# Performance work log

Hardware: AMD Instinct MI355X
Metric: run time of the kernel (lower is better)

The kernel has to match this reference:

```python
import jax, jax.numpy as jnp
import numpy as np

N_NODES = 500_000
N_EDGES = 1_000_000
EMB = 64           # config.Model.embedding_size
F = 128            # config.Model.latency_feature_size
L = 8              # config.Latency.latency_feature_length
OP_CNT = 5000
SV_CNT = 2000
ST_CNT = 16
IN_DIM = 3 * EMB + L  # 200


def setup_inputs() -> dict:
    key = jax.random.key(0)
    ks = jax.random.split(key, 24)
    s = 0.02
    inp = {
        'operation_id': jax.random.randint(ks[0], (N_NODES,), 0, OP_CNT, dtype=jnp.int32),
        'service_id':   jax.random.randint(ks[1], (N_NODES,), 0, SV_CNT, dtype=jnp.int32),
        'status_id':    jax.random.randint(ks[2], (N_NODES,), 0, ST_CNT, dtype=jnp.int32),
        'latency_feat': jax.random.normal(ks[3], (N_NODES, L), dtype=jnp.float32),
        'edge_src':     jax.random.randint(ks[4], (N_EDGES,), 0, N_NODES, dtype=jnp.int32),
        'edge_dst':     jax.random.randint(ks[5], (N_EDGES,), 0, N_NODES, dtype=jnp.int32),
        'eps':          jax.random.normal(ks[6], (N_NODES, F), dtype=jnp.float32),
        # parameters (LevelEmbedding + TreeLSTMLatencyEncoder + TreeLSTMLatencyDecoder)
        'op_embed':      jax.random.normal(ks[7],  (OP_CNT, EMB), dtype=jnp.float32) * s,
        'service_embed': jax.random.normal(ks[8],  (SV_CNT, EMB), dtype=jnp.float32) * s,
        'status_embed':  jax.random.normal(ks[9],  (ST_CNT, EMB), dtype=jnp.float32) * s,
        'enc_W1': jax.random.normal(ks[10], (IN_DIM, F), dtype=jnp.float32) * s,
        'enc_b1': jnp.zeros((F,), dtype=jnp.float32),
        'enc_W2': jax.random.normal(ks[11], (F, 2 * F), dtype=jnp.float32) * s,
        'enc_b2': jnp.zeros((2 * F,), dtype=jnp.float32),
        'dec_Wself': jax.random.normal(ks[12], (F, F), dtype=jnp.float32) * s,
        'dec_Wagg':  jax.random.normal(ks[13], (F, F), dtype=jnp.float32) * s,
        'mu_W': jax.random.normal(ks[14], (F, L), dtype=jnp.float32) * s,
        'mu_b': jnp.zeros((L,), dtype=jnp.float32),
        'lv_W': jax.random.normal(ks[15], (F, L), dtype=jnp.float32) * s,
        'lv_b': jnp.zeros((L,), dtype=jnp.float32),
        'opwise_embed': jax.random.normal(ks[16], (OP_CNT + 1, 2 * L * L), dtype=jnp.float32) * s,
    }
    return inp


def reference(operation_id, service_id, status_id, latency_feat, edge_src, edge_dst, eps,
              op_embed, service_embed, status_embed,
              enc_W1, enc_b1, enc_W2, enc_b2,
              dec_Wself, dec_Wagg, mu_W, mu_b, lv_W, lv_b, opwise_embed):
    N = latency_feat.shape[0]
    # ---- LevelEmbedding: gathers + concat ----
    feats = jnp.concatenate([
        op_embed[operation_id],
        service_embed[service_id],
        status_embed[status_id],
        latency_feat,
    ], axis=-1)  # [N, 3*EMB + L]
    # ---- TreeLSTMLatencyEncoder ----
    h = jax.nn.relu(feats @ enc_W1 + enc_b1)
    y = h @ enc_W2 + enc_b2                       # [N, 2F]
    z_mu, z_lv = jnp.split(y, 2, axis=-1)
    z_lv = jnp.tanh(z_lv)
    z = z_mu + jnp.exp(0.5 * z_lv) * eps          # reparameterize, [N, F]
    # ---- TreeLSTM decoder (one child-sum message-passing step over edges) ----
    agg = jax.ops.segment_sum(z[edge_src], edge_dst, num_segments=N)  # scatter-reduce
    yd = jax.nn.relu(z @ dec_Wself + agg @ dec_Wagg)                  # [N, F]
    mu = yd @ mu_W + mu_b   # [N, L]
    lv = yd @ lv_W + lv_b   # [N, L]
    # op-wise output transform: per-node [1,L] @ [L,L]
    w = opwise_embed[operation_id].reshape(N, L, 2 * L)
    w_mu, w_lv = w[..., :L], w[..., L:]
    mu = jnp.einsum('nl,nlk->nk', mu, w_mu)
    lv = jnp.einsum('nl,nlk->nk', lv, w_lv)
    # ---- latency_loss: gaussian NLL + opid scatter aggregation ----
    label = latency_feat
    loss = (mu - label) ** 2 / (2.0 * jnp.exp(lv) + 1e-7) + 0.5 * lv  # [N, L]
    loss_node = jnp.mean(loss, axis=1)                                 # [N]
    op_loss = jax.ops.segment_sum(loss_node, operation_id, num_segments=OP_CNT)
    op_cnt = jax.ops.segment_sum(jnp.ones((N,), jnp.int32), operation_id, num_segments=OP_CNT)
    lat_loss = jnp.mean(loss_node)
    kl = -0.5 * jnp.mean(z_lv + 1.0 - jnp.exp(z_lv) - z_mu ** 2)
    total = lat_loss + kl
    return (total, op_loss, op_cnt)
```

## Files before the change

kernel.cpp:

```cpp
#include <hip/hip_runtime.h>
#include <math.h>

#define NN 500000
#define NE 1000000
#define OPC 5000
#define NBLK_SCAN 489
#define NBLK ((NN + 127) / 128)

typedef short short8 __attribute__((ext_vector_type(8)));
typedef float f32x4 __attribute__((ext_vector_type(4)));

static __device__ __forceinline__ short f2bf(float f) {
    unsigned u = __builtin_bit_cast(unsigned, f);
    u += 0x7fffu + ((u >> 16) & 1u);
    return (short)(u >> 16);
}
static __device__ __forceinline__ float bf2f(short s) {
    unsigned u = ((unsigned)(unsigned short)s) << 16;
    return __builtin_bit_cast(float, u);
}
static __device__ __forceinline__ short8 cvt8(float4 a, float4 b) {
    short8 r;
    r[0] = f2bf(a.x); r[1] = f2bf(a.y); r[2] = f2bf(a.z); r[3] = f2bf(a.w);
    r[4] = f2bf(b.x); r[5] = f2bf(b.y); r[6] = f2bf(b.z); r[7] = f2bf(b.w);
    return r;
}
static __device__ __forceinline__ short8 ldcvt(const float* p) {
    const float4* p4 = (const float4*)p;
    return cvt8(p4[0], p4[1]);
}

__global__ void prep_kernel(const float* __restrict__ W1, const float* __restrict__ W2,
                            const float* __restrict__ Wself, const float* __restrict__ Wagg,
                            const float* __restrict__ muW, const float* __restrict__ lvW,
                            short* __restrict__ W1f, short* __restrict__ W2f,
                            short* __restrict__ Wf0, short* __restrict__ Wf1,
                            short* __restrict__ HWf)
{
    int idx = blockIdx.x * 256 + threadIdx.x;
    int j = idx & 7, lane = (idx >> 3) & 63;
    int m = lane & 15, q = lane >> 4;
    {
        int s = idx >> 12, nf = (idx >> 9) & 7;
        int k = s * 32 + q * 8 + j, col = nf * 16 + m;
        W1f[idx] = (k < 200) ? f2bf(W1[k * 128 + col]) : (short)0;
    }
    {
        int s = idx >> 13, nf = (idx >> 9) & 15;
        int k = s * 32 + q * 8 + j, col = nf * 16 + m;
        W2f[idx] = f2bf(W2[k * 256 + col]);
    }
    if (idx < 16384) {
        int s = idx >> 12, nf = (idx >> 9) & 7;
        int k = s * 32 + q * 8 + j, col = nf * 16 + m;
        Wf0[idx] = f2bf(Wself[k * 128 + col]);
        Wf1[idx] = f2bf(Wagg[k * 128 + col]);
    }
    if (idx < 2048) {
        int k = (idx >> 9) * 32 + q * 8 + j;
        HWf[idx] = (m < 8) ? f2bf(muW[k * 8 + m]) : f2bf(lvW[k * 8 + (m - 8)]);
    }
}

__global__ __launch_bounds__(256, 4) void enc1_mfma(
    const int* __restrict__ op_id, const int* __restrict__ sv_id, const int* __restrict__ st_id,
    const float* __restrict__ lat,
    const float* __restrict__ opE, const float* __restrict__ svE, const float* __restrict__ stE,
    const short* __restrict__ W1f, const float* __restrict__ b1,
    short* __restrict__ h_bf)
{
    __shared__ __align__(16) short Hs[128 * 136];
    const int tid = threadIdx.x;
    const int lane = tid & 63, w = tid >> 6;
    const int m = lane & 15, q = lane >> 4;
    const int bbase = blockIdx.x * 128;
    const int wbase = bbase + w * 32;
    const bool wv = (wbase < NN);

    #pragma unroll
    for (int a2 = 0; a2 < 2; a2++) {
        if (wv) {
            const int n0 = wbase + a2 * 16 + m;
            const size_t op0 = (size_t)op_id[n0] * 64;
            const size_t sv0 = (size_t)sv_id[n0] * 64;
            const size_t st0 = (size_t)st_id[n0] * 64;

            f32x4 acc[8];
            #pragma unroll
            for (int nf = 0; nf < 8; nf++) acc[nf] = (f32x4)0.0f;

            #pragma unroll
            for (int s = 0; s < 7; s++) {
                short8 a0;
                if (s < 2)      a0 = ldcvt(opE + op0 + s * 32 + q * 8);
                else if (s < 4) a0 = ldcvt(svE + sv0 + (s - 2) * 32 + q * 8);
                else if (s < 6) a0 = ldcvt(stE + st0 + (s - 4) * 32 + q * 8);
                else {
                    if (q == 0) a0 = ldcvt(lat + (size_t)n0 * 8);
                    else {
                        #pragma unroll
                        for (int i = 0; i < 8; i++) a0[i] = 0;
                    }
                }
                #pragma unroll
                for (int nf = 0; nf < 8; nf++) {
                    const short8 b = *(const short8*)(W1f + (s * 8 + nf) * 512 + lane * 8);
                    acc[nf] = __builtin_amdgcn_mfma_f32_16x16x32_bf16(a0, b, acc[nf], 0, 0, 0);
                }
            }
            #pragma unroll
            for (int nf = 0; nf < 8; nf++) {
                int col = nf * 16 + m;
                float bb = b1[col];
                #pragma unroll
                for (int r = 0; r < 4; r++) {
                    int g = w * 32 + a2 * 16 + q * 4 + r;
                    Hs[g * 136 + col] = f2bf(fmaxf(acc[nf][r] + bb, 0.0f));
                }
            }
        }
    }
    __syncthreads();

    {
        int g = tid >> 1, cb = (tid & 1) * 64;
        int node = bbase + g;
        if (node < NN) {
            short8* dst = (short8*)(h_bf + (size_t)node * 128 + cb);
            const short8* src = (const short8*)&Hs[g * 136 + cb];
            #pragma unroll
            for (int i = 0; i < 8; i++) dst[i] = src[i];
        }
    }
}

__global__ __launch_bounds__(256, 4) void enc2_mfma(
    const short* __restrict__ h_bf, const short* __restrict__ W2f, const float* __restrict__ b2,
    const float* __restrict__ eps, short* __restrict__ z_bf, float* __restrict__ kl_sum)
{
    __shared__ __align__(16) int ldsI[64 * 132];
    const int tid = threadIdx.x;
    const int lane = tid & 63, w = tid >> 6;
    const int m = lane & 15, q = lane >> 4;
    const int bbase = blockIdx.x * 128;
    const int wbase = bbase + w * 32;
    const bool wv = (wbase < NN);

    float kll = 0.0f;
    #pragma unroll
    for (int a2 = 0; a2 < 2; a2++) {
        if (wv) {
            short8 a[4];
            #pragma unroll
            for (int s = 0; s < 4; s++)
                a[s] = *(const short8*)(h_bf + (size_t)(wbase + a2 * 16 + m) * 128 + s * 32 + q * 8);

            f32x4 acc[16];
            #pragma unroll
            for (int nf = 0; nf < 16; nf++) acc[nf] = (f32x4)0.0f;

            #pragma unroll
            for (int s = 0; s < 4; s++) {
                #pragma unroll
                for (int nf = 0; nf < 16; nf++) {
                    const short8 b = *(const short8*)(W2f + (s * 16 + nf) * 512 + lane * 8);
                    acc[nf] = __builtin_amdgcn_mfma_f32_16x16x32_bf16(a[s], b, acc[nf], 0, 0, 0);
                }
            }

            #pragma unroll
            for (int nf = 0; nf < 8; nf++) {
                int col = nf * 16 + m;
                float bm = b2[col], bl = b2[col + 128];
                #pragma unroll
                for (int r = 0; r < 4; r++) {
                    float mu = acc[nf][r] + bm;
                    float lr = acc[nf + 8][r] + bl;
                    float e2 = __expf(2.0f * lr);
                    float t  = 1.0f - 2.0f * __builtin_amdgcn_rcpf(e2 + 1.0f);
                    float s  = __expf(0.5f * t);
                    kll += t + 1.0f - s * s - mu * mu;
                    int pk = (int)(unsigned short)f2bf(mu)
                           | ((int)(unsigned short)f2bf(s) << 16);
                    ldsI[(w * 16 + q * 4 + r) * 132 + col] = pk;
                }
            }
        }
        __syncthreads();
        {
            int g = tid >> 2, cb = (tid & 3) * 32;
            int node = bbase + (g >> 4) * 32 + a2 * 16 + (g & 15);
            if (node < NN) {
                const float4* ep = (const float4*)(eps + (size_t)node * 128 + cb);
                const int4*   lp = (const int4*)&ldsI[g * 132 + cb];
                #pragma unroll
                for (int c = 0; c < 4; c++) {
                    int4 va = lp[c * 2], vb = lp[c * 2 + 1];
                    float4 ea = ep[c * 2], eb = ep[c * 2 + 1];
                    short8 o;
                    o[0] = f2bf(fmaf(bf2f((short)(va.x >> 16)), ea.x, bf2f((short)va.x)));
                    o[1] = f2bf(fmaf(bf2f((short)(va.y >> 16)), ea.y, bf2f((short)va.y)));
                    o[2] = f2bf(fmaf(bf2f((short)(va.z >> 16)), ea.z, bf2f((short)va.z)));
                    o[3] = f2bf(fmaf(bf2f((short)(va.w >> 16)), ea.w, bf2f((short)va.w)));
                    o[4] = f2bf(fmaf(bf2f((short)(vb.x >> 16)), eb.x, bf2f((short)vb.x)));
                    o[5] = f2bf(fmaf(bf2f((short)(vb.y >> 16)), eb.y, bf2f((short)vb.y)));
                    o[6] = f2bf(fmaf(bf2f((short)(vb.z >> 16)), eb.z, bf2f((short)vb.z)));
                    o[7] = f2bf(fmaf(bf2f((short)(vb.w >> 16)), eb.w, bf2f((short)vb.w)));
                    *(short8*)(z_bf + (size_t)node * 128 + cb + c * 8) = o;
                }
            }
        }
        __syncthreads();
    }
    #pragma unroll
    for (int off = 32; off > 0; off >>= 1) kll += __shfl_down(kll, off);
    if (lane == 0) atomicAdd(kl_sum, kll);
}

__global__ void hist_kernel(const int* __restrict__ edst, int* __restrict__ cnt)
{
    int e = blockIdx.x * 256 + threadIdx.x;
    if (e < NE) atomicAdd(&cnt[edst[e]], 1);
}

__global__ void scan1_kernel(const int* __restrict__ cnt, int* __restrict__ bsum)
{
    __shared__ int ls[256];
    int b = blockIdx.x, tid = threadIdx.x;
    int idx0 = b * 1024 + tid * 4;
    int s = 0;
    #pragma unroll
    for (int i = 0; i < 4; i++) { int idx = idx0 + i; if (idx < NN) s += cnt[idx]; }
    ls[tid] = s; __syncthreads();
    for (int off = 128; off > 0; off >>= 1) {
        if (tid < off) ls[tid] += ls[tid + off];
        __syncthreads();
    }
    if (tid == 0) bsum[b] = ls[0];
}

__global__ void scan2_kernel(int* __restrict__ bsum, int* __restrict__ rowstart)
{
    __shared__ int ls[512];
    int tid = threadIdx.x;
    int v = (tid < NBLK_SCAN) ? bsum[tid] : 0;
    ls[tid] = v; __syncthreads();
    for (int off = 1; off < 512; off <<= 1) {
        int t = 0;
        if (tid >= off) t = ls[tid - off];
        __syncthreads();
        ls[tid] += t;
        __syncthreads();
    }
    if (tid < NBLK_SCAN) bsum[tid] = (tid == 0) ? 0 : ls[tid - 1];
    if (tid == 0) rowstart[NN] = NE;
}

__global__ void scan3_kernel(const int* __restrict__ cnt, const int* __restrict__ bsum,
                             int* __restrict__ rowstart, int* __restrict__ cursor)
{
    __shared__ int ls[256];
    int b = blockIdx.x, tid = threadIdx.x;
    int idx0 = b * 1024 + tid * 4;
    int v[4]; int s = 0;
    #pragma unroll
    for (int i = 0; i < 4; i++) { int idx = idx0 + i; v[i] = (idx < NN) ? cnt[idx] : 0; s += v[i]; }
    ls[tid] = s; __syncthreads();
    for (int off = 1; off < 256; off <<= 1) {
        int t = 0;
        if (tid >= off) t = ls[tid - off];
        __syncthreads();
        ls[tid] += t;
        __syncthreads();
    }
    int ex = ls[tid] - s + bsum[b];
    #pragma unroll
    for (int i = 0; i < 4; i++) {
        int idx = idx0 + i;
        if (idx < NN) { rowstart[idx] = ex; cursor[idx] = ex; }
        ex += v[i];
    }
}

__global__ void fill_kernel(const int* __restrict__ esrc, const int* __restrict__ edst,
                            int* __restrict__ cursor, int* __restrict__ csr)
{
    int e = blockIdx.x * 256 + threadIdx.x;
    if (e < NE) {
        int pos = atomicAdd(&cursor[edst[e]], 1);
        csr[pos] = esrc[e];
    }
}

__global__ __launch_bounds__(256, 4) void dec_mfma(
    const short* __restrict__ z_bf, const int* __restrict__ rowstart, const int* __restrict__ csr,
    const short* __restrict__ Wf0, const short* __restrict__ Wf1, const short* __restrict__ HWf,
    const float* __restrict__ mub, const float* __restrict__ lvb,
    const float* __restrict__ opwise, const int* __restrict__ op_id,
    const float* __restrict__ lat,
    float* __restrict__ op_loss, float* __restrict__ op_cnt,
    float* __restrict__ loss_sum)
{
    __shared__ __align__(16) short regionA[128 * 128];
    float* mlv = (float*)regionA;

    const int tid = threadIdx.x;
    const int lane = tid & 63, w = tid >> 6;
    const int m = lane & 15, q = lane >> 4;
    const int bbase = blockIdx.x * 128;
    const int wbase = bbase + w * 32;
    const bool wv = (wbase < NN);

    #pragma unroll
    for (int half = 0; half < 2; half++) {
        int nodeL = half * 64 + (tid >> 2);
        int chunk = tid & 3;
        int n = bbase + nodeL;
        float a[32];
        #pragma unroll
        for (int i = 0; i < 32; i++) a[i] = 0.0f;
        if (n < NN) {
            int r0 = rowstart[n], r1 = rowstart[n + 1];
            for (int e = r0; e < r1; e++) {
                const short8* zp = (const short8*)(z_bf + (size_t)csr[e] * 128 + chunk * 32);
                #pragma unroll
                for (int j = 0; j < 4; j++) {
                    short8 v = zp[j];
                    #pragma unroll
                    for (int i = 0; i < 8; i++) a[j * 8 + i] += bf2f(v[i]);
                }
            }
        }
        #pragma unroll
        for (int j = 0; j < 4; j++) {
            int c = chunk * 4 + j;
            int slot = (c ^ (nodeL & 7)) * 8;
            short8 o;
            #pragma unroll
            for (int i = 0; i < 8; i++) o[i] = f2bf(a[j * 8 + i]);
            *(short8*)&regionA[nodeL * 128 + slot] = o;
        }
    }
    __syncthreads();

    f32x4 h0[2];
    h0[0] = (f32x4)0.0f; h0[1] = (f32x4)0.0f;

    if (wv) {
        #pragma unroll
        for (int a2 = 0; a2 < 2; a2++) {
            short8 az[4];
            #pragma unroll
            for (int s = 0; s < 4; s++)
                az[s] = *(const short8*)(z_bf + (size_t)(wbase + a2 * 16 + m) * 128 + s * 32 + q * 8);

            f32x4 acc[8];
            #pragma unroll
            for (int nf = 0; nf < 8; nf++) acc[nf] = (f32x4)0.0f;

            #pragma unroll
            for (int s = 0; s < 4; s++) {
                #pragma unroll
                for (int nf = 0; nf < 8; nf++) {
                    const short8 b = *(const short8*)(Wf0 + (s * 8 + nf) * 512 + lane * 8);
                    acc[nf] = __builtin_amdgcn_mfma_f32_16x16x32_bf16(az[s], b, acc[nf], 0, 0, 0);
                }
            }

            #pragma unroll
            for (int s = 0; s < 4; s++) {
                const int slot = ((4 * s + q) ^ (m & 7)) * 8;
                const short8 a0 = *(const short8*)&regionA[(w * 32 + a2 * 16 + m) * 128 + slot];
                #pragma unroll
                for (int nf = 0; nf < 8; nf++) {
                    const short8 b = *(const short8*)(Wf1 + (s * 8 + nf) * 512 + lane * 8);
                    acc[nf] = __builtin_amdgcn_mfma_f32_16x16x32_bf16(a0, b, acc[nf], 0, 0, 0);
                }
            }

            #pragma unroll
            for (int nf = 0; nf < 8; nf++) {
                int c = nf * 2 + (m >> 3);
                #pragma unroll
                for (int r = 0; r < 4; r++) {
                    int node = w * 32 + a2 * 16 + q * 4 + r;
                    regionA[node * 128 + ((c ^ (node & 7)) * 8) + (m & 7)] =
                        f2bf(fmaxf(acc[nf][r], 0.0f));
                }
            }

            #pragma unroll
            for (int s2 = 0; s2 < 4; s2++) {
                const int slot = ((4 * s2 + q) ^ (m & 7)) * 8;
                short8 a0 = *(const short8*)&regionA[(w * 32 + a2 * 16 + m) * 128 + slot];
                short8 b  = *(const short8*)(HWf + s2 * 512 + lane * 8);
                h0[a2] = __builtin_amdgcn_mfma_f32_16x16x32_bf16(a0, b, h0[a2], 0, 0, 0);
            }
        }
    }
    __syncthreads();

    if (wv) {
        float hb = (m < 8) ? mub[m] : lvb[m - 8];
        #pragma unroll
        for (int a2 = 0; a2 < 2; a2++)
            #pragma unroll
            for (int r = 0; r < 4; r++)
                mlv[(w * 32 + a2 * 16 + q * 4 + r) * 17 + m] = h0[a2][r] + hb;
    }
    __syncthreads();

    float lsum = 0.0f;
    if (tid < 128 && bbase + tid < NN) {
        const int t = tid;
        const int n = bbase + t;
        const int op = op_id[n];
        const float4* w4 = (const float4*)(opwise + (size_t)op * 128);
        float mout[8], lout[8];
        #pragma unroll
        for (int k = 0; k < 8; k++) { mout[k] = 0.0f; lout[k] = 0.0f; }
        #pragma unroll
        for (int l = 0; l < 8; l++) {
            float mv = mlv[t * 17 + l];
            float vv = mlv[t * 17 + 8 + l];
            float4 a = w4[l * 4 + 0];
            float4 b = w4[l * 4 + 1];
            float4 c = w4[l * 4 + 2];
            float4 d = w4[l * 4 + 3];
            mout[0] = fmaf(mv, a.x, mout[0]); mout[1] = fmaf(mv, a.y, mout[1]);
            mout[2] = fmaf(mv, a.z, mout[2]); mout[3] = fmaf(mv, a.w, mout[3]);
            mout[4] = fmaf(mv, b.x, mout[4]); mout[5] = fmaf(mv, b.y, mout[5]);
            mout[6] = fmaf(mv, b.z, mout[6]); mout[7] = fmaf(mv, b.w, mout[7]);
            lout[0] = fmaf(vv, c.x, lout[0]); lout[1] = fmaf(vv, c.y, lout[1]);
            lout[2] = fmaf(vv, c.z, lout[2]); lout[3] = fmaf(vv, c.w, lout[3]);
            lout[4] = fmaf(vv, d.x, lout[4]); lout[5] = fmaf(vv, d.y, lout[5]);
            lout[6] = fmaf(vv, d.z, lout[6]); lout[7] = fmaf(vv, d.w, lout[7]);
        }
        const float4* lp = (const float4*)(lat + (size_t)n * 8);
        float4 lb0 = lp[0], lb1 = lp[1];
        float labels[8] = {lb0.x, lb0.y, lb0.z, lb0.w, lb1.x, lb1.y, lb1.z, lb1.w};
        float lnode = 0.0f;
        #pragma unroll
        for (int k = 0; k < 8; k++) {
            float diff = mout[k] - labels[k];
            lnode += diff * diff / (2.0f * expf(lout[k]) + 1e-7f) + 0.5f * lout[k];
        }
        lnode *= 0.125f;
        atomicAdd(&op_loss[op], lnode);
        atomicAdd(&op_cnt[op], 1.0f);
        lsum = lnode;
    }
    #pragma unroll
    for (int off = 32; off > 0; off >>= 1) lsum += __shfl_down(lsum, off);
    if (lane == 0) atomicAdd(loss_sum, lsum);
}

__global__ void final_kernel(const float* __restrict__ accum, float* __restrict__ out)
{
    out[0] = accum[1] / (float)NN - 0.5f * (accum[0] / (float)((size_t)NN * 128));
}

extern "C" void kernel_launch(void* const* d_in, const int* in_sizes, int n_in,
                              void* d_out, int out_size, void* d_ws, size_t ws_size,
                              hipStream_t stream) {
    const int*   op_id  = (const int*)  d_in[0];
    const int*   sv_id  = (const int*)  d_in[1];
    const int*   st_id  = (const int*)  d_in[2];
    const float* lat    = (const float*)d_in[3];
    const int*   esrc   = (const int*)  d_in[4];
    const int*   edst   = (const int*)  d_in[5];
    const float* eps    = (const float*)d_in[6];
    const float* opE    = (const float*)d_in[7];
    const float* svE    = (const float*)d_in[8];
    const float* stE    = (const float*)d_in[9];
    const float* W1     = (const float*)d_in[10];
    const float* b1     = (const float*)d_in[11];
    const float* W2     = (const float*)d_in[12];
    const float* b2     = (const float*)d_in[13];
    const float* Wself  = (const float*)d_in[14];
    const float* Wagg   = (const float*)d_in[15];
    const float* muW    = (const float*)d_in[16];
    const float* mub    = (const float*)d_in[17];
    const float* lvW    = (const float*)d_in[18];
    const float* lvb    = (const float*)d_in[19];
    const float* opwise = (const float*)d_in[20];

    char* wsb = (char*)d_ws;
    short* W1f      = (short*)(wsb + 0);
    short* W2f      = (short*)(wsb + 65536);
    short* Wf0      = (short*)(wsb + 131072);
    short* Wf1      = (short*)(wsb + 163840);
    short* HWf      = (short*)(wsb + 196608);
    float* accum    = (float*)(wsb + 204800);
    int*   cnt      = (int*)  (wsb + (4  << 20));
    int*   rowstart = (int*)  (wsb + (6  << 20));
    int*   cursor   = (int*)  (wsb + (9  << 20));
    int*   csr      = (int*)  (wsb + (12 << 20));
    int*   bsum     = (int*)  (wsb + (16 << 20));
    short* h_bf     = (short*)(wsb + (32  << 20));
    short* z_bf     = (short*)(wsb + (160ull << 20));
    float* out      = (float*)d_out;

    hipMemsetAsync(d_out, 0, (size_t)out_size * sizeof(float), stream);
    hipMemsetAsync(accum, 0, 2 * sizeof(float), stream);
    hipMemsetAsync(cnt, 0, (size_t)NN * sizeof(int), stream);

    prep_kernel<<<128, 256, 0, stream>>>(W1, W2, Wself, Wagg, muW, lvW,
                                         W1f, W2f, Wf0, Wf1, HWf);

    hist_kernel<<<(NE + 255) / 256, 256, 0, stream>>>(edst, cnt);
    scan1_kernel<<<NBLK_SCAN, 256, 0, stream>>>(cnt, bsum);
    scan2_kernel<<<1, 512, 0, stream>>>(bsum, rowstart);
    scan3_kernel<<<NBLK_SCAN, 256, 0, stream>>>(cnt, bsum, rowstart, cursor);
    fill_kernel<<<(NE + 255) / 256, 256, 0, stream>>>(esrc, edst, cursor, csr);

    enc1_mfma<<<NBLK, 256, 0, stream>>>(op_id, sv_id, st_id, lat, opE, svE, stE, W1f, b1, h_bf);
    enc2_mfma<<<NBLK, 256, 0, stream>>>(h_bf, W2f, b2, eps, z_bf, accum + 0);
    dec_mfma<<<NBLK, 256, 0, stream>>>(z_bf, rowstart, csr, Wf0, Wf1, HWf, mub, lvb,
                                       opwise, op_id, lat,
                                       out + 1, out + 1 + OPC, accum + 1);
    final_kernel<<<1, 1, 0, stream>>>(accum, out);
}
```

Before: 1.196 ms.

## Stage encoder weight fragments through LDS and share B loads across row tiles

In enc1, the W1 fragments are now copied cooperatively into LDS in two chunks, and each wave computes both 16-row tiles at once, so every B fragment read feeds two MFMAs. In enc2, W2 is likewise staged through LDS in two halves, reusing the same region as the output staging buffer. The aim is to replace repeated per-wave global (L2) weight reads with LDS reads. The cost is extra __syncthreads barriers, doubled accumulator registers in enc1, and in enc2 the weight tile is reloaded into LDS for each a2 iteration.

```diff
diff --git a/kernel.cpp b/kernel.cpp
--- a/kernel.cpp
+++ b/kernel.cpp
@@ -69,7 +69,10 @@
     const short* __restrict__ W1f, const float* __restrict__ b1,
     short* __restrict__ h_bf)
 {
-    __shared__ __align__(16) short Hs[128 * 136];
+    __shared__ __align__(16) char region[34816];
+    short* Wb = (short*)region;
+    short* Hs = (short*)region;
+
     const int tid = threadIdx.x;
     const int lane = tid & 63, w = tid >> 6;
     const int m = lane & 15, q = lane >> 4;
@@ -77,47 +80,95 @@
     const int wbase = bbase + w * 32;
     const bool wv = (wbase < NN);
 
-    #pragma unroll
-    for (int a2 = 0; a2 < 2; a2++) {
-        if (wv) {
-            const int n0 = wbase + a2 * 16 + m;
-            const size_t op0 = (size_t)op_id[n0] * 64;
-            const size_t sv0 = (size_t)sv_id[n0] * 64;
-            const size_t st0 = (size_t)st_id[n0] * 64;
-
-            f32x4 acc[8];
-            #pragma unroll
-            for (int nf = 0; nf < 8; nf++) acc[nf] = (f32x4)0.0f;
-
-            #pragma unroll
-            for (int s = 0; s < 7; s++) {
-                short8 a0;
-                if (s < 2)      a0 = ldcvt(opE + op0 + s * 32 + q * 8);
-                else if (s < 4) a0 = ldcvt(svE + sv0 + (s - 2) * 32 + q * 8);
-                else if (s < 6) a0 = ldcvt(stE + st0 + (s - 4) * 32 + q * 8);
-                else {
-                    if (q == 0) a0 = ldcvt(lat + (size_t)n0 * 8);
-                    else {
-                        #pragma unroll
-                        for (int i = 0; i < 8; i++) a0[i] = 0;
-                    }
-                }
-                #pragma unroll
-                for (int nf = 0; nf < 8; nf++) {
-                    const short8 b = *(const short8*)(W1f + (s * 8 + nf) * 512 + lane * 8);
-                    acc[nf] = __builtin_amdgcn_mfma_f32_16x16x32_bf16(a0, b, acc[nf], 0, 0, 0);
-                }
+    f32x4 acc[2][8];
+    #pragma unroll
+    for (int a2 = 0; a2 < 2; a2++)
+        #pragma unroll
+        for (int nf = 0; nf < 8; nf++) acc[a2][nf] = (f32x4)0.0f;
+
+    int n0i = 0, n1i = 0;
+    size_t op0 = 0, op1 = 0, sv0 = 0, sv1 = 0, st0 = 0, st1 = 0;
+    if (wv) {
+        n0i = wbase + m; n1i = wbase + 16 + m;
+        op0 = (size_t)op_id[n0i] * 64; op1 = (size_t)op_id[n1i] * 64;
+        sv0 = (size_t)sv_id[n0i] * 64; sv1 = (size_t)sv_id[n1i] * 64;
+        st0 = (size_t)st_id[n0i] * 64; st1 = (size_t)st_id[n1i] * 64;
+    }
+
+    {
+        const short8* g = (const short8*)W1f;
+        short8* l = (short8*)Wb;
+        #pragma unroll
+        for (int i = 0; i < 8; i++) l[tid + 256 * i] = g[tid + 256 * i];
+    }
+    __syncthreads();
+    if (wv) {
+        #pragma unroll
+        for (int s = 0; s < 4; s++) {
+            short8 a0, a1;
+            if (s < 2) {
+                a0 = ldcvt(opE + op0 + s * 32 + q * 8);
+                a1 = ldcvt(opE + op1 + s * 32 + q * 8);
+            } else {
+                a0 = ldcvt(svE + sv0 + (s - 2) * 32 + q * 8);
+                a1 = ldcvt(svE + sv1 + (s - 2) * 32 + q * 8);
             }
             #pragma unroll
             for (int nf = 0; nf < 8; nf++) {
-                int col = nf * 16 + m;
-                float bb = b1[col];
+                const short8 b = *(const short8*)(Wb + (s * 8 + nf) * 512 + lane * 8);
+                acc[0][nf] = __builtin_amdgcn_mfma_f32_16x16x32_bf16(a0, b, acc[0][nf], 0, 0, 0);
+                acc[1][nf] = __builtin_amdgcn_mfma_f32_16x16x32_bf16(a1, b, acc[1][nf], 0, 0, 0);
+            }
+        }
+    }
+    __syncthreads();
+
+    {
+        const short8* g = (const short8*)(W1f + 16384);
+        short8* l = (short8*)Wb;
+        #pragma unroll
+        for (int i = 0; i < 6; i++) l[tid + 256 * i] = g[tid + 256 * i];
+    }
+    __syncthreads();
+    if (wv) {
+        #pragma unroll
+        for (int s = 4; s < 7; s++) {
+            short8 a0, a1;
+            if (s < 6) {
+                a0 = ldcvt(stE + st0 + (s - 4) * 32 + q * 8);
+                a1 = ldcvt(stE + st1 + (s - 4) * 32 + q * 8);
+            } else {
+                if (q == 0) {
+                    a0 = ldcvt(lat + (size_t)n0i * 8);
+                    a1 = ldcvt(lat + (size_t)n1i * 8);
+                } else {
+                    #pragma unroll
+                    for (int i = 0; i < 8; i++) { a0[i] = 0; a1[i] = 0; }
+                }
+            }
+            const int sl = s - 4;
+            #pragma unroll
+            for (int nf = 0; nf < 8; nf++) {
+                const short8 b = *(const short8*)(Wb + (sl * 8 + nf) * 512 + lane * 8);
+                acc[0][nf] = __builtin_amdgcn_mfma_f32_16x16x32_bf16(a0, b, acc[0][nf], 0, 0, 0);
+                acc[1][nf] = __builtin_amdgcn_mfma_f32_16x16x32_bf16(a1, b, acc[1][nf], 0, 0, 0);
+            }
+        }
+    }
+    __syncthreads();
+
+    if (wv) {
+        #pragma unroll
+        for (int nf = 0; nf < 8; nf++) {
+            int col = nf * 16 + m;
+            float bb = b1[col];
+            #pragma unroll
+            for (int a2 = 0; a2 < 2; a2++)
                 #pragma unroll
                 for (int r = 0; r < 4; r++) {
                     int g = w * 32 + a2 * 16 + q * 4 + r;
-                    Hs[g * 136 + col] = f2bf(fmaxf(acc[nf][r] + bb, 0.0f));
-                }
-            }
+                    Hs[g * 136 + col] = f2bf(fmaxf(acc[a2][nf][r] + bb, 0.0f));
+                }
         }
     }
     __syncthreads();
@@ -138,7 +189,10 @@
     const short* __restrict__ h_bf, const short* __restrict__ W2f, const float* __restrict__ b2,
     const float* __restrict__ eps, short* __restrict__ z_bf, float* __restrict__ kl_sum)
 {
-    __shared__ __align__(16) int ldsI[64 * 132];
+    __shared__ __align__(16) char region[33792];
+    short* Wb = (short*)region;
+    int* ldsI = (int*)region;
+
     const int tid = threadIdx.x;
     const int lane = tid & 63, w = tid >> 6;
     const int m = lane & 15, q = lane >> 4;
@@ -149,25 +203,54 @@
     float kll = 0.0f;
     #pragma unroll
     for (int a2 = 0; a2 < 2; a2++) {
+        short8 a[4];
         if (wv) {
-            short8 a[4];
             #pragma unroll
             for (int s = 0; s < 4; s++)
                 a[s] = *(const short8*)(h_bf + (size_t)(wbase + a2 * 16 + m) * 128 + s * 32 + q * 8);
-
-            f32x4 acc[16];
-            #pragma unroll
-            for (int nf = 0; nf < 16; nf++) acc[nf] = (f32x4)0.0f;
-
-            #pragma unroll
-            for (int s = 0; s < 4; s++) {
+        }
+
+        f32x4 acc[16];
+        #pragma unroll
+        for (int nf = 0; nf < 16; nf++) acc[nf] = (f32x4)0.0f;
+
+        {
+            const short8* g8 = (const short8*)W2f;
+            short8* l = (short8*)Wb;
+            #pragma unroll
+            for (int i = 0; i < 8; i++) l[tid + 256 * i] = g8[tid + 256 * i];
+        }
+        __syncthreads();
+        if (wv) {
+            #pragma unroll
+            for (int sl = 0; sl < 2; sl++)
                 #pragma unroll
                 for (int nf = 0; nf < 16; nf++) {
-                    const short8 b = *(const short8*)(W2f + (s * 16 + nf) * 512 + lane * 8);
-                    acc[nf] = __builtin_amdgcn_mfma_f32_16x16x32_bf16(a[s], b, acc[nf], 0, 0, 0);
-                }
-            }
-
+                    const short8 b = *(const short8*)(Wb + (sl * 16 + nf) * 512 + lane * 8);
+                    acc[nf] = __builtin_amdgcn_mfma_f32_16x16x32_bf16(a[sl], b, acc[nf], 0, 0, 0);
+                }
+        }
+        __syncthreads();
+
+        {
+            const short8* g8 = (const short8*)(W2f + 16384);
+            short8* l = (short8*)Wb;
+            #pragma unroll
+            for (int i = 0; i < 8; i++) l[tid + 256 * i] = g8[tid + 256 * i];
+        }
+        __syncthreads();
+        if (wv) {
+            #pragma unroll
+            for (int sl = 0; sl < 2; sl++)
+                #pragma unroll
+                for (int nf = 0; nf < 16; nf++) {
+                    const short8 b = *(const short8*)(Wb + (sl * 16 + nf) * 512 + lane * 8);
+                    acc[nf] = __builtin_amdgcn_mfma_f32_16x16x32_bf16(a[sl + 2], b, acc[nf], 0, 0, 0);
+                }
+        }
+        __syncthreads();
+
+        if (wv) {
             #pragma unroll
             for (int nf = 0; nf < 8; nf++) {
                 int col = nf * 16 + m;
```

Result: faster. 1.059 ms (-11.4%).
